# Optimization experiments

Hardware: AMD Instinct MI355X
Metric: run time of the kernel (lower is better)

The kernel has to match this reference:

```python
import jax, jax.numpy as jnp
import numpy as np

B, T, C = 4, 2048, 1024
H, DQK, DV = 16, 64, 64
W_SCALE = 0.02  # keep logits in a sane range (mimics GPT-style init)


def setup_inputs() -> dict:
    key = jax.random.key(0)
    k1, k2, k3, k4, k5 = jax.random.split(key, 5)
    x = jax.random.normal(k1, (B, T, C), dtype=jnp.float32)
    Wq = jax.random.normal(k2, (C, H * DQK), dtype=jnp.float32) * W_SCALE
    Wk = jax.random.normal(k3, (C, H * DQK), dtype=jnp.float32) * W_SCALE
    Wv = jax.random.normal(k4, (C, H * DV), dtype=jnp.float32) * W_SCALE
    Wp = jax.random.normal(k5, (DV, C), dtype=jnp.float32) * W_SCALE
    return {"x": x, "Wq": Wq, "Wk": Wk, "Wv": Wv, "Wp": Wp, "iter_num": 0}


def reference(x, Wq, Wk, Wv, Wp, iter_num):
    b, t, c = x.shape
    # projections, split into heads: [B, H, T, D]
    q = (x @ Wq).reshape(b, t, H, DQK).transpose(0, 2, 1, 3)
    k = (x @ Wk).reshape(b, t, H, DQK).transpose(0, 2, 1, 3)
    v = (x @ Wv).reshape(b, t, H, DV).transpose(0, 2, 1, 3)
    scale = 1.0 / jnp.sqrt(jnp.asarray(DQK, dtype=x.dtype))
    att = jnp.einsum('bhqd,bhkd->bhqk', q, k) * scale  # [B,H,T,T]
    causal = jnp.tril(jnp.ones((t, t), dtype=bool))
    att = jnp.where(causal[None, None, :, :], att, -jnp.inf)
    att = jax.nn.softmax(att, axis=-1)
    # att @ v then SUM over heads (not concat): [B, T, DV]
    y = jnp.einsum('bhqk,bhkd->bqd', att, v)
    return y @ Wp  # [B, T, C]
```

## Files before the change

### kernel.cpp

```cpp
#include <hip/hip_runtime.h>
#include <hip/hip_bf16.h>

#define DEVI __device__ __forceinline__

typedef __bf16 bf16x8 __attribute__((ext_vector_type(8)));
typedef float f32x4 __attribute__((ext_vector_type(4)));

DEVI unsigned short f2bf(float x) {
    union { __hip_bfloat16 h; unsigned short u; } v;
    v.h = __float2bfloat16(x);
    return v.u;
}

DEVI float exp2_fast(float x) {
#if __has_builtin(__builtin_amdgcn_exp2f)
    return __builtin_amdgcn_exp2f(x);
#else
    return exp2f(x);
#endif
}

DEVI void gload16(const void* gsrc, void* lds) {
    __builtin_amdgcn_global_load_lds(
        (const __attribute__((address_space(1))) void*)gsrc,
        (__attribute__((address_space(3))) void*)lds,
        16, 0, 0);
}

#define BARRIER_MEM() asm volatile("s_barrier" ::: "memory")
#define WAITVM(n) asm volatile("s_waitcnt vmcnt(" #n ")" ::: "memory")


__global__ __launch_bounds__(256) void convert_f32_bf16_vec(
    const float* __restrict__ in, unsigned short* __restrict__ out, int n4) {
    int i = blockIdx.x * 256 + threadIdx.x;
    if (i >= n4) return;
    float4 v = reinterpret_cast<const float4*>(in)[i];
    ushort4 o;
    o.x = f2bf(v.x); o.y = f2bf(v.y); o.z = f2bf(v.z); o.w = f2bf(v.w);
    reinterpret_cast<ushort4*>(out)[i] = o;
}

__global__ __launch_bounds__(256) void transpose_wqkv(
    const float* __restrict__ wq, const float* __restrict__ wk,
    const float* __restrict__ wv, unsigned short* __restrict__ dst) {
    __shared__ unsigned short tile[32][33];
    const float* src = (blockIdx.z == 0) ? wq : (blockIdx.z == 1) ? wk : wv;
    unsigned short* d = dst + blockIdx.z * 1024 * 1024;
    int c0 = blockIdx.x * 32, r0 = blockIdx.y * 32;
    int tx = threadIdx.x & 31, ty = threadIdx.x >> 5;
    #pragma unroll
    for (int i = ty; i < 32; i += 8)
        tile[tx][i] = f2bf(src[(r0 + i) * 1024 + c0 + tx]);
    __syncthreads();
    #pragma unroll
    for (int i = ty; i < 32; i += 8)
        d[(c0 + i) * 1024 + r0 + tx] = tile[i][tx];
}

__global__ __launch_bounds__(256) void transpose_f32_to_bf16t(
    const float* __restrict__ src, unsigned short* __restrict__ dst,
    int R, int Cc) {
    __shared__ unsigned short tile[32][33];
    int c0 = blockIdx.x * 32, r0 = blockIdx.y * 32;
    int tx = threadIdx.x & 31, ty = threadIdx.x >> 5;
    #pragma unroll
    for (int i = ty; i < 32; i += 8)
        tile[tx][i] = f2bf(src[(r0 + i) * Cc + c0 + tx]);
    __syncthreads();
    #pragma unroll
    for (int i = ty; i < 32; i += 8)
        dst[(c0 + i) * R + r0 + tx] = tile[i][tx];
}

__global__ __launch_bounds__(256) void transpose_v(
    const unsigned short* __restrict__ vp, unsigned short* __restrict__ vt) {
    __shared__ unsigned short tile[32][33];
    int bh = blockIdx.x;
    int t0 = blockIdx.y * 32;
    int d0 = blockIdx.z * 32;
    int b = bh >> 4, h = bh & 15;
    int tx = threadIdx.x & 31, ty = threadIdx.x >> 5;
    #pragma unroll
    for (int i = ty; i < 32; i += 8)
        tile[tx][i] = vp[(b * 2048 + t0 + i) * 1024 + h * 64 + d0 + tx];
    __syncthreads();
    #pragma unroll
    for (int i = ty; i < 32; i += 8)
        vt[(bh * 64 + d0 + i) * 2048 + t0 + tx] = tile[i][tx];
}

template <int EPI>
__global__ __launch_bounds__(256) void gemm_bt(
    const unsigned short* __restrict__ A, const unsigned short* __restrict__ Bt,
    int Mdim, int Ndim, int Kdim,
    unsigned short* __restrict__ q_out, unsigned short* __restrict__ k_out,
    unsigned short* __restrict__ v_out, float* __restrict__ c_out) {
    __shared__ unsigned short As[128 * 32];
    __shared__ unsigned short Bs[128 * 32];
    const int ntn = Ndim >> 7;
    const int bm = (blockIdx.x / ntn) << 7;
    const int bn = (blockIdx.x % ntn) << 7;
    const int tid = threadIdx.x;
    const int w = tid >> 6, l = tid & 63;
    const int wr = w >> 1, wc = w & 1;
    const int lrow = l >> 2, lcb = (l & 3) * 8;
    const int lc = l & 15, lg = l >> 4;

    f32x4 acc[4][4] = {};

    for (int k0 = 0; k0 < Kdim; k0 += 32) {
        __syncthreads();
        #pragma unroll
        for (int i = 0; i < 2; ++i) {
            int j = w * 2 + i;
            gload16(A + (bm + j * 16 + lrow) * Kdim + k0 + lcb, (char*)As + j * 1024);
            gload16(Bt + (bn + j * 16 + lrow) * Kdim + k0 + lcb, (char*)Bs + j * 1024);
        }
        __syncthreads();
        bf16x8 af[4], bfr[4];
        #pragma unroll
        for (int mi = 0; mi < 4; ++mi)
            af[mi] = *reinterpret_cast<const bf16x8*>(&As[(wr * 64 + mi * 16 + lc) * 32 + lg * 8]);
        #pragma unroll
        for (int ni = 0; ni < 4; ++ni)
            bfr[ni] = *reinterpret_cast<const bf16x8*>(&Bs[(wc * 64 + ni * 16 + lc) * 32 + lg * 8]);
        #pragma unroll
        for (int mi = 0; mi < 4; ++mi)
            #pragma unroll
            for (int ni = 0; ni < 4; ++ni)
                acc[mi][ni] = __builtin_amdgcn_mfma_f32_16x16x32_bf16(
                    af[mi], bfr[ni], acc[mi][ni], 0, 0, 0);
    }

    #pragma unroll
    for (int mi = 0; mi < 4; ++mi) {
        #pragma unroll
        for (int ni = 0; ni < 4; ++ni) {
            #pragma unroll
            for (int r = 0; r < 4; ++r) {
                int m = bm + wr * 64 + mi * 16 + lg * 4 + r;
                int n = bn + wc * 64 + ni * 16 + lc;
                float val = acc[mi][ni][r];
                if (EPI == 0) {
                    int which = n >> 10, rr = n & 1023;
                    unsigned short* dst = (which == 0) ? q_out : (which == 1) ? k_out : v_out;
                    dst[m * 1024 + rr] = f2bf(val);
                } else {
                    c_out[m * Ndim + n] = val;
                }
            }
        }
    }
}

__global__ __launch_bounds__(512, 4) void attn_kernel(
    const unsigned short* __restrict__ qb, const unsigned short* __restrict__ kb,
    const unsigned short* __restrict__ vt, unsigned short* __restrict__ ypart) {
    __shared__ unsigned short Ks[2][64 * 64];
    __shared__ unsigned short Vs[2][64 * 64];
    __shared__ unsigned short plds[8][16 * 72];

    const int i = blockIdx.x;
    const int slot = i >> 3;
    const int bh = (i & 7) + ((slot >> 3) << 3);
    const int pr = slot & 7;
    const int b = bh >> 4, h = bh & 15;
    const int tid = threadIdx.x, w = tid >> 6, l = tid & 63;
    const int lc = l & 15, lg = l >> 4;

    const float SCL = 0.125f * 1.44269504f;

    const int rowc = l >> 3;
    const int colsw = 8 * ((l & 7) ^ rowc);
    const unsigned short* kbh = kb + (b * 2048) * 1024 + h * 64;
    const unsigned short* vbh = vt + bh * 64 * 2048;

    const int swz = (lc & 7) * 8;

    unsigned short* pl = &plds[w][0];

    auto STAGE = [&](int bufn, int kt) {
        const int tk0s = kt << 6;
        const int row = w * 8 + rowc;
        gload16(kbh + (tk0s + row) * 1024 + colsw, (char*)&Ks[bufn][0] + w * 1024);
        gload16(vbh + row * 2048 + tk0s + colsw, (char*)&Vs[bufn][0] + w * 1024);
    };

    auto run_pass = [&](int qblk) {
        const int q0 = qblk << 7;
        const int qrowW = q0 + w * 16;

        bf16x8 qf[2];
        {
            const unsigned short* qp =
                qb + (b * 2048 + qrowW + lc) * 1024 + h * 64;
            qf[0] = *reinterpret_cast<const bf16x8*>(qp + lg * 8);
            qf[1] = *reinterpret_cast<const bf16x8*>(qp + 32 + lg * 8);
        }

        f32x4 accO[4] = {};
        float lsum[4] = {};

        const int nkt = 2 * qblk + 2;
        STAGE(0, 0);

        for (int kt = 0; kt < nkt; ++kt) {
            const int cur = kt & 1;
            const int tk0 = kt << 6;
            if (kt + 1 < nkt) {
                STAGE(cur ^ 1, kt + 1);
                WAITVM(2);
            } else {
                WAITVM(0);
            }
            BARRIER_MEM();

            if (tk0 <= qrowW + 15) {
                f32x4 s[4] = {};
                #pragma unroll
                for (int ni = 0; ni < 4; ++ni) {
                    const unsigned short* kr = &Ks[cur][(ni * 16 + lc) * 64];
                    bf16x8 kf0 = *reinterpret_cast<const bf16x8*>(&kr[(lg * 8) ^ swz]);
                    bf16x8 kf1 = *reinterpret_cast<const bf16x8*>(&kr[(32 + lg * 8) ^ swz]);
                    s[ni] = __builtin_amdgcn_mfma_f32_16x16x32_bf16(qf[0], kf0, s[ni], 0, 0, 0);
                    s[ni] = __builtin_amdgcn_mfma_f32_16x16x32_bf16(qf[1], kf1, s[ni], 0, 0, 0);
                }
                const bool needmask = (tk0 + 63 > qrowW);
                #pragma unroll
                for (int ni = 0; ni < 4; ++ni) {
                    #pragma unroll
                    for (int r = 0; r < 4; ++r) {
                        float sv = s[ni][r] * SCL;
                        if (needmask) {
                            int tq = qrowW + lg * 4 + r;
                            int tk = tk0 + ni * 16 + lc;
                            sv = (tk > tq) ? -INFINITY : sv;
                        }
                        float pv = exp2_fast(sv);
                        lsum[r] += pv;
                        pl[(lg * 4 + r) * 72 + ni * 16 + lc] = f2bf(pv);
                    }
                }
                bf16x8 pf0 = *reinterpret_cast<const bf16x8*>(&pl[lc * 72 + lg * 8]);
                bf16x8 pf1 = *reinterpret_cast<const bf16x8*>(&pl[lc * 72 + 32 + lg * 8]);
                #pragma unroll
                for (int ni = 0; ni < 4; ++ni) {
                    const unsigned short* vr = &Vs[cur][(ni * 16 + lc) * 64];
                    bf16x8 vf0 = *reinterpret_cast<const bf16x8*>(&vr[(lg * 8) ^ swz]);
                    bf16x8 vf1 = *reinterpret_cast<const bf16x8*>(&vr[(32 + lg * 8) ^ swz]);
                    accO[ni] = __builtin_amdgcn_mfma_f32_16x16x32_bf16(pf0, vf0, accO[ni], 0, 0, 0);
                    accO[ni] = __builtin_amdgcn_mfma_f32_16x16x32_bf16(pf1, vf1, accO[ni], 0, 0, 0);
                }
            }
            BARRIER_MEM();
        }

        #pragma unroll
        for (int r = 0; r < 4; ++r) {
            float t = lsum[r];
            #pragma unroll
            for (int msk = 1; msk <= 8; msk <<= 1)
                t += __shfl_xor(t, msk);
            float rinv = 1.0f / t;
            int tq = qrowW + lg * 4 + r;
            #pragma unroll
            for (int ni = 0; ni < 4; ++ni)
                ypart[(bh * 2048 + tq) * 64 + ni * 16 + lc] =
                    f2bf(accO[ni][r] * rinv);
        }
    };

    run_pass(15 - pr);
    run_pass(pr);
}

__global__ __launch_bounds__(256) void reduce_heads(
    const unsigned short* __restrict__ ypart, unsigned short* __restrict__ yb) {
    int idx = blockIdx.x * 256 + threadIdx.x;
    int d = idx & 63, m = idx >> 6;
    int b = m >> 11, t = m & 2047;
    const unsigned short* p = ypart + ((b * 16) * 2048 + t) * 64 + d;
    float s = 0.f;
    #pragma unroll
    for (int h = 0; h < 16; ++h) {
        union { unsigned short u; __hip_bfloat16 h; } v;
        v.u = p[h * 2048 * 64];
        s += __bfloat162float(v.h);
    }
    yb[idx] = f2bf(s);
}


extern "C" void kernel_launch(void* const* d_in, const int* in_sizes, int n_in,
                              void* d_out, int out_size, void* d_ws, size_t ws_size,
                              hipStream_t stream) {
    const float* x  = (const float*)d_in[0];
    const float* Wq = (const float*)d_in[1];
    const float* Wk = (const float*)d_in[2];
    const float* Wv = (const float*)d_in[3];
    const float* Wp = (const float*)d_in[4];
    float* out = (float*)d_out;

    if (ws_size < 91357184) return;
    char* ws = (char*)d_ws;
    unsigned short* ypart = (unsigned short*)ws;
    unsigned short* xb   = (unsigned short*)ws;
    unsigned short* vprj = (unsigned short*)(ws + 16777216);
    unsigned short* wt   = (unsigned short*)(ws + 33554432);
    unsigned short* wpt  = (unsigned short*)(ws + 39845888);
    unsigned short* qbf  = (unsigned short*)(ws + 39976960);
    unsigned short* kbf  = (unsigned short*)(ws + 56754176);
    unsigned short* vtb  = (unsigned short*)(ws + 73531392);
    unsigned short* yb   = (unsigned short*)(ws + 90308608);

    convert_f32_bf16_vec<<<8192, 256, 0, stream>>>(x, xb, 2097152);
    transpose_wqkv<<<dim3(32, 32, 3), 256, 0, stream>>>(Wq, Wk, Wv, wt);
    transpose_f32_to_bf16t<<<dim3(32, 2), 256, 0, stream>>>(Wp, wpt, 64, 1024);

    gemm_bt<0><<<(8192 / 128) * (3072 / 128), 256, 0, stream>>>(
        xb, wt, 8192, 3072, 1024, qbf, kbf, vprj, nullptr);

    transpose_v<<<dim3(64, 64, 2), 256, 0, stream>>>(vprj, vtb);

    attn_kernel<<<512, 512, 0, stream>>>(qbf, kbf, vtb, ypart);

    reduce_heads<<<2048, 256, 0, stream>>>(ypart, yb);

    gemm_bt<1><<<(8192 / 128) * (1024 / 128), 256, 0, stream>>>(
        yb, wpt, 8192, 1024, 64, nullptr, nullptr, nullptr, out);
}
```

Before: 177.4 us.

## Replace QKV projection GEMM with 256x256-tile double-buffered pipelined kernel

The QKV projection GEMM moves from a 128x128-tile, 256-thread kernel to a new 256x256-tile, 512-thread kernel with a BK=64 double buffer. The new kernel loads into LDS directly from global memory and interleaves staging of later K tiles with quadrant-wise MFMA compute, raising MFMA priority around the compute. It also remaps block indices across 8 groups to improve cache locality. The aim is more data reuse per LDS load and overlap of loads with compute in the largest GEMM. In exchange it uses more registers and 128KB of LDS per block, and its many barriers make the schedule fragile.

```diff
diff --git a/kernel.cpp b/kernel.cpp
--- a/kernel.cpp
+++ b/kernel.cpp
@@ -29,6 +29,7 @@
 
 #define BARRIER_MEM() asm volatile("s_barrier" ::: "memory")
 #define WAITVM(n) asm volatile("s_waitcnt vmcnt(" #n ")" ::: "memory")
+#define LGKM0() asm volatile("s_waitcnt lgkmcnt(0)" ::: "memory")
 
 
 __global__ __launch_bounds__(256) void convert_f32_bf16_vec(
@@ -88,6 +89,123 @@
     #pragma unroll
     for (int i = ty; i < 32; i += 8)
         vt[(bh * 64 + d0 + i) * 2048 + t0 + tx] = tile[i][tx];
+}
+
+#define LOAD_A8(mh) do { \
+    _Pragma("unroll") \
+    for (int q = 0; q < 4; ++q) { \
+        a[q][0] = *(const bf16x8*)(Arow + ((mh) * 64 + q * 16) * 128 + p16_0); \
+        a[q][1] = *(const bf16x8*)(Arow + ((mh) * 64 + q * 16) * 128 + p16_1); \
+    } } while (0)
+
+#define LOAD_B4(nh) do { \
+    _Pragma("unroll") \
+    for (int q2 = 0; q2 < 2; ++q2) { \
+        b##nh[q2][0] = *(const bf16x8*)(Brow + ((nh) * 32 + q2 * 16) * 128 + p16_0); \
+        b##nh[q2][1] = *(const bf16x8*)(Brow + ((nh) * 32 + q2 * 16) * 128 + p16_1); \
+    } } while (0)
+
+#define QUAD(mh, nh) do { \
+    __builtin_amdgcn_s_setprio(1); \
+    _Pragma("unroll") \
+    for (int q = 0; q < 4; ++q) { \
+        _Pragma("unroll") \
+        for (int q2 = 0; q2 < 2; ++q2) { \
+            acc[(mh) * 4 + q][(nh) * 2 + q2] = __builtin_amdgcn_mfma_f32_16x16x32_bf16( \
+                a[q][0], b##nh[q2][0], acc[(mh) * 4 + q][(nh) * 2 + q2], 0, 0, 0); \
+            acc[(mh) * 4 + q][(nh) * 2 + q2] = __builtin_amdgcn_mfma_f32_16x16x32_bf16( \
+                a[q][1], b##nh[q2][1], acc[(mh) * 4 + q][(nh) * 2 + q2], 0, 0, 0); \
+        } } \
+    __builtin_amdgcn_s_setprio(0); } while (0)
+
+__global__ __launch_bounds__(512, 2) void gemm256(
+    const unsigned short* __restrict__ A, const unsigned short* __restrict__ Bt,
+    unsigned short* __restrict__ q_out, unsigned short* __restrict__ k_out,
+    unsigned short* __restrict__ v_out) {
+    __shared__ unsigned short Ab[2][256 * 64];
+    __shared__ unsigned short Bb[2][256 * 64];
+
+    const int wg = (blockIdx.x & 7) * 48 + (blockIdx.x >> 3);
+    const int bm = (wg / 12) << 8;
+    const int bn = (wg % 12) << 8;
+
+    const int tid = threadIdx.x;
+    const int w = tid >> 6, l = tid & 63;
+    const int wm = w >> 2, wn = w & 3;
+    const int lc = l & 15, lg = l >> 4;
+    const int lr8 = l >> 3;
+    const int colsw = 8 * ((l & 7) ^ lr8);
+
+    const unsigned short* gA = A + (size_t)(bm + lr8) * 1024 + colsw;
+    const unsigned short* gB = Bt + (size_t)(bn + lr8) * 1024 + colsw;
+
+    const int p16_0 = ((lg) ^ (lc & 7)) * 16;
+    const int p16_1 = ((4 | lg) ^ (lc & 7)) * 16;
+
+    auto STAGE_A = [&](int h, int bufn, int tt) {
+        #pragma unroll
+        for (int j = 0; j < 2; ++j) {
+            const int row0 = wm * 128 + h * 64 + ((((w & 3) << 1) | j) << 3);
+            gload16(gA + row0 * 1024 + tt * 64, (char*)&Ab[bufn][0] + row0 * 128);
+        }
+    };
+    auto STAGE_B = [&](int g, int bufn, int tt) {
+        #pragma unroll
+        for (int j = 0; j < 2; ++j) {
+            const int row0 = (w >> 1) * 64 + g * 32 + ((((w & 1) << 1) | j) << 3);
+            gload16(gB + row0 * 1024 + tt * 64, (char*)&Bb[bufn][0] + row0 * 128);
+        }
+    };
+
+    bf16x8 a[4][2], b0[2][2], b1[2][2];
+    f32x4 acc[8][4] = {};
+
+    const int nt = 16;
+
+    STAGE_A(0, 0, 0); STAGE_B(0, 0, 0); STAGE_B(1, 0, 0); STAGE_A(1, 0, 0);
+    STAGE_A(0, 1, 1); STAGE_B(0, 1, 1); STAGE_B(1, 1, 1);
+
+    #pragma unroll 1
+    for (int t = 0; t < nt; ++t) {
+        const int buf = t & 1;
+        const char* Arow = (const char*)&Ab[buf][0] + (wm * 128 + lc) * 128;
+        const char* Brow = (const char*)&Bb[buf][0] + (wn * 64 + lc) * 128;
+        if (t == nt - 1) { WAITVM(0); } else { WAITVM(6); }
+        BARRIER_MEM();
+        LOAD_A8(0);
+        LOAD_B4(0);
+        if (t + 1 < nt) STAGE_A(1, buf ^ 1, t + 1);
+        BARRIER_MEM(); LGKM0();
+        QUAD(0, 0);
+        BARRIER_MEM();
+        LOAD_B4(1);
+        if (t + 2 < nt) STAGE_A(0, buf, t + 2);
+        BARRIER_MEM(); LGKM0();
+        QUAD(0, 1);
+        BARRIER_MEM();
+        LOAD_A8(1);
+        if (t + 2 < nt) STAGE_B(0, buf, t + 2);
+        BARRIER_MEM(); LGKM0();
+        QUAD(1, 1);
+        BARRIER_MEM();
+        if (t + 2 < nt) STAGE_B(1, buf, t + 2);
+        BARRIER_MEM();
+        QUAD(1, 0);
+    }
+
+    const int whichsel = bn >> 10;
+    unsigned short* dst = (whichsel == 0) ? q_out : (whichsel == 1) ? k_out : v_out;
+    const int rrbase = (bn & 1023) + wn * 64 + lc;
+    #pragma unroll
+    for (int mi = 0; mi < 8; ++mi) {
+        #pragma unroll
+        for (int r = 0; r < 4; ++r) {
+            const int m = bm + wm * 128 + mi * 16 + lg * 4 + r;
+            #pragma unroll
+            for (int ni = 0; ni < 4; ++ni)
+                dst[(size_t)m * 1024 + rrbase + ni * 16] = f2bf(acc[mi][ni][r]);
+        }
+    }
 }
 
 template <int EPI>
@@ -175,7 +293,6 @@
     const int colsw = 8 * ((l & 7) ^ rowc);
     const unsigned short* kbh = kb + (b * 2048) * 1024 + h * 64;
     const unsigned short* vbh = vt + bh * 64 * 2048;
-
     const int swz = (lc & 7) * 8;
 
     unsigned short* pl = &plds[w][0];
@@ -318,8 +435,7 @@
     transpose_wqkv<<<dim3(32, 32, 3), 256, 0, stream>>>(Wq, Wk, Wv, wt);
     transpose_f32_to_bf16t<<<dim3(32, 2), 256, 0, stream>>>(Wp, wpt, 64, 1024);
 
-    gemm_bt<0><<<(8192 / 128) * (3072 / 128), 256, 0, stream>>>(
-        xb, wt, 8192, 3072, 1024, qbf, kbf, vprj, nullptr);
+    gemm256<<<384, 512, 0, stream>>>(xb, wt, qbf, kbf, vprj);
 
     transpose_v<<<dim3(64, 64, 2), 256, 0, stream>>>(vprj, vtb);
 
```

After: 169.3 us. -4.6%, faster.
